# Performance work log

Measured on AMD Instinct MI355X. Metric: run time of the kernel, lower is better.

Reference implementation:

```python
import jax, jax.numpy as jnp
import numpy as np

D_MODEL = 1024
D_K = 1024
B, T = 4, 2048


def setup_inputs() -> dict:
    key = jax.random.key(0)
    kx, kq, kk, kv = jax.random.split(key, 4)
    s = 1.0 / np.sqrt(D_MODEL)
    return {
        "x": jax.random.normal(kx, (B, T, D_MODEL), dtype=jnp.float32),
        "W_q": jax.random.normal(kq, (D_MODEL, D_K), dtype=jnp.float32) * s,
        "W_k": jax.random.normal(kk, (D_MODEL, D_K), dtype=jnp.float32) * s,
        "W_v": jax.random.normal(kv, (D_MODEL, D_K), dtype=jnp.float32) * s,
    }


def reference(x, W_q, W_k, W_v):
    # x: (B, T, C); W_*: (C, d_k). Linear(no bias) == x @ W
    q = jnp.einsum('btc,ck->btk', x, W_q)
    k = jnp.einsum('btc,ck->btk', x, W_k)
    v = jnp.einsum('btc,ck->btk', x, W_v)
    d_k = W_q.shape[1]
    scores = jnp.einsum('bqk,bsk->bqs', q, k) / jnp.sqrt(jnp.asarray(d_k, x.dtype))
    T_ = x.shape[1]
    causal = jnp.tril(jnp.ones((T_, T_), dtype=bool))
    scores = jnp.where(causal, scores, jnp.asarray(-jnp.inf, scores.dtype))
    weights = jax.nn.softmax(scores, axis=-1)
    return jnp.einsum('bqs,bsk->bqk', weights, v)
```

## Files before the change

### kernel.cpp

```cpp
#include <hip/hip_runtime.h>
#include <hip/hip_bf16.h>
#include <stdint.h>

typedef __bf16 bf16x8 __attribute__((ext_vector_type(8)));
typedef float  f32x4  __attribute__((ext_vector_type(4)));
typedef unsigned int u32x4 __attribute__((ext_vector_type(4)));

__device__ __forceinline__ unsigned short f2bf(float x) {
    union { float f; unsigned u; } v; v.f = x;
    unsigned r = v.u + 0x7fffu + ((v.u >> 16) & 1u);
    return (unsigned short)(r >> 16);
}

__device__ __forceinline__ void async16(const void* g, void* l) {
    __builtin_amdgcn_global_load_lds(
        (const __attribute__((address_space(1))) void*)g,
        (__attribute__((address_space(3))) void*)l,
        16, 0, 0);
}

template <typename OutT, bool CAUSAL_SKIP, bool KLIMIT>
__global__ __launch_bounds__(256, 3) void gemm_bt(
    const unsigned short* __restrict__ A,
    const unsigned short* __restrict__ Bt,
    OutT* __restrict__ C,
    int M, int N, int K, int lda, int ldb, int ldc,
    long long sA, long long sB, long long sC, float scale)
{
    const int bn = blockIdx.x, bm = blockIdx.y, bz = blockIdx.z;
    if (CAUSAL_SKIP && bn > bm) return;

    A  += (long long)bz * sA;
    Bt += (long long)bz * sB;
    C  += (long long)bz * sC;

    const int m0 = bm * 128, n0 = bn * 128;
    const int Keff = KLIMIT ? min(K, (bm + 1) * 128) : K;

    __shared__ __align__(16) unsigned short LDS[2 * 2 * 128 * 32];

    const int tid  = threadIdx.x;
    const int w    = tid >> 6, l = tid & 63;
    const int wr   = w >> 1,  wc = w & 1;
    const int lrow = l & 15,  quad = l >> 4;

    f32x4 acc[4][4] = {};

    const int rA0  = 32 * w + (l >> 2);
    const int cOff = (((l & 3) ^ ((l >> 3) & 3))) * 8;
    const unsigned short* aG0 = A  + (long long)(m0 + rA0)      * lda + cOff;
    const unsigned short* aG1 = A  + (long long)(m0 + rA0 + 16) * lda + cOff;
    const unsigned short* bG0 = Bt + (long long)(n0 + rA0)      * ldb + cOff;
    const unsigned short* bG1 = Bt + (long long)(n0 + rA0 + 16) * ldb + cOff;
    unsigned short* aL = &LDS[(2 * w) * 512 + l * 8];
    unsigned short* bL = aL + 4096;

    const int sl = (lrow >> 1) & 3;

    async16(aG0, aL);
    async16(aG1, aL + 512);
    async16(bG0, bL);
    async16(bG1, bL + 512);

    for (int k0 = 0; k0 < Keff; k0 += 32) {
        const int cur = ((k0 >> 5) & 1) * 8192;
        __syncthreads();

        if (k0 + 32 < Keff) {
            const int nxt = cur ^ 8192;
            async16(aG0 + k0 + 32, aL + nxt);
            async16(aG1 + k0 + 32, aL + nxt + 512);
            async16(bG0 + k0 + 32, bL + nxt);
            async16(bG1 + k0 + 32, bL + nxt + 512);
        }

        const unsigned short* As = &LDS[cur];
        const unsigned short* Bs = &LDS[cur + 4096];
        bf16x8 af[4], bfr[4];
#pragma unroll
        for (int i = 0; i < 4; i++) {
            af[i]  = *(const bf16x8*)&As[(wr * 64 + i * 16 + lrow) * 32 + (quad ^ sl) * 8];
            bfr[i] = *(const bf16x8*)&Bs[(wc * 64 + i * 16 + lrow) * 32 + (quad ^ sl) * 8];
        }
#pragma unroll
        for (int i = 0; i < 4; i++)
#pragma unroll
            for (int j = 0; j < 4; j++)
                acc[i][j] = __builtin_amdgcn_mfma_f32_16x16x32_bf16(af[i], bfr[j], acc[i][j], 0, 0, 0);
    }
    __syncthreads();

    char* eb = (char*)LDS + w * 2288;
    const int erow = l >> 2, ep = l & 3;

    if constexpr (sizeof(OutT) == 2) {
#pragma unroll
        for (int i = 0; i < 4; i++) {
#pragma unroll
            for (int j = 0; j < 4; j++)
#pragma unroll
                for (int r = 0; r < 4; r++)
                    *(unsigned short*)(eb + (quad * 4 + r) * 144 + (j * 16 + lrow) * 2) =
                        f2bf(acc[i][j][r] * scale);
            const long long gm = m0 + wr * 64 + i * 16 + erow;
#pragma unroll
            for (int c = 0; c < 2; c++) {
                u32x4 d = *(u32x4*)(eb + erow * 144 + ep * 32 + c * 16);
                *(u32x4*)((unsigned short*)C + gm * ldc + (n0 + wc * 64 + ep * 16 + c * 8)) = d;
            }
        }
    } else {
#pragma unroll
        for (int i = 0; i < 4; i++) {
            const long long gm = m0 + wr * 64 + i * 16 + erow;
#pragma unroll
            for (int jc = 0; jc < 2; jc++) {
#pragma unroll
                for (int jj = 0; jj < 2; jj++)
#pragma unroll
                    for (int r = 0; r < 4; r++)
                        *(float*)(eb + (quad * 4 + r) * 144 + (jj * 16 + lrow) * 4) =
                            acc[i][2 * jc + jj][r] * scale;
#pragma unroll
                for (int c = 0; c < 2; c++) {
                    f32x4 d = *(f32x4*)(eb + erow * 144 + ep * 32 + c * 16);
                    *(f32x4*)((float*)C + gm * ldc + (n0 + wc * 64 + jc * 32 + ep * 8 + c * 4)) = d;
                }
            }
        }
    }
}

__global__ __launch_bounds__(256) void cast_f32_bf16(
    const float4* __restrict__ in, unsigned short* __restrict__ out, int n4)
{
    int i = blockIdx.x * 256 + threadIdx.x;
    if (i >= n4) return;
    float4 v = in[i];
    union { unsigned short u[4]; uint2 p; } o;
    o.u[0] = f2bf(v.x); o.u[1] = f2bf(v.y); o.u[2] = f2bf(v.z); o.u[3] = f2bf(v.w);
    *(uint2*)(out + (long long)i * 4) = o.p;
}

__global__ __launch_bounds__(256) void transpose_cast_w3(
    const float* __restrict__ W0, const float* __restrict__ W1,
    const float* __restrict__ W2, unsigned short* __restrict__ out, int n)
{
    const float* in = (blockIdx.z == 0) ? W0 : (blockIdx.z == 1) ? W1 : W2;
    out += (long long)blockIdx.z * n * n;
    __shared__ float tile[32][33];
    const int tx = threadIdx.x, ty = threadIdx.y;
    const int c0 = blockIdx.x * 32, r0 = blockIdx.y * 32;
#pragma unroll
    for (int i = 0; i < 4; i++)
        tile[ty + i * 8][tx] = in[(long long)(r0 + ty + i * 8) * n + c0 + tx];
    __syncthreads();
#pragma unroll
    for (int i = 0; i < 4; i++)
        out[(long long)(c0 + ty + i * 8) * n + r0 + tx] = f2bf(tile[tx][ty + i * 8]);
}

__global__ __launch_bounds__(256) void transpose_bf16_k(
    const unsigned short* __restrict__ in, unsigned short* __restrict__ out,
    int ldin, int ldout, long long sin, long long sout)
{
    in  += (long long)blockIdx.z * sin;
    out += (long long)blockIdx.z * sout;
    __shared__ unsigned short tile[32][33];
    const int tx = threadIdx.x, ty = threadIdx.y;
    const int c0 = blockIdx.x * 32, r0 = blockIdx.y * 32;
#pragma unroll
    for (int i = 0; i < 4; i++)
        tile[ty + i * 8][tx] = in[(long long)(r0 + ty + i * 8) * ldin + c0 + tx];
    __syncthreads();
#pragma unroll
    for (int i = 0; i < 4; i++)
        out[(long long)(c0 + ty + i * 8) * ldout + r0 + tx] = tile[tx][ty + i * 8];
}

__global__ __launch_bounds__(256) void causal_softmax(
    const float* __restrict__ S, unsigned short* __restrict__ P, int T)
{
    const int row = blockIdx.x;
    const int t   = row & (T - 1);
    const float* s = S + (long long)row * T;
    unsigned short* p = P + (long long)row * T;
    const int L = t + 1;
    const int tid = threadIdx.x;

    float v[8];
    float mx = -3.0e38f;
#pragma unroll
    for (int k = 0; k < 8; k++) {
        const int j = tid + k * 256;
        v[k] = (j < L) ? s[j] : -3.0e38f;
        mx = fmaxf(mx, v[k]);
    }
#pragma unroll
    for (int off = 32; off; off >>= 1) mx = fmaxf(mx, __shfl_xor(mx, off));
    __shared__ float red[4], red2[4];
    const int wid = tid >> 6, lid = tid & 63;
    if (lid == 0) red[wid] = mx;
    __syncthreads();
    mx = fmaxf(fmaxf(red[0], red[1]), fmaxf(red[2], red[3]));

    float sum = 0.f;
#pragma unroll
    for (int k = 0; k < 8; k++) { v[k] = __expf(v[k] - mx); sum += v[k]; }
#pragma unroll
    for (int off = 32; off; off >>= 1) sum += __shfl_xor(sum, off);
    if (lid == 0) red2[wid] = sum;
    __syncthreads();
    sum = red2[0] + red2[1] + red2[2] + red2[3];
    const float inv = 1.0f / sum;
#pragma unroll
    for (int k = 0; k < 8; k++) {
        const int j = tid + k * 256;
        p[j] = f2bf(v[k] * inv);
    }
}

extern "C" void kernel_launch(void* const* d_in, const int* in_sizes, int n_in,
                              void* d_out, int out_size, void* d_ws, size_t ws_size,
                              hipStream_t stream)
{
    const int B = 4, T = 2048, C = 1024, D = 1024;
    const float* x  = (const float*)d_in[0];
    const float* Wq = (const float*)d_in[1];
    const float* Wk = (const float*)d_in[2];
    const float* Wv = (const float*)d_in[3];
    float* out = (float*)d_out;
    char* ws = (char*)d_ws;

    const size_t MB = 1ull << 20;
    unsigned short* Xbf   = (unsigned short*)(ws + 0);
    unsigned short* WqkvT = (unsigned short*)(ws + 16 * MB);
    unsigned short* QKV   = (unsigned short*)(ws + 22 * MB);
    unsigned short* Vt    = (unsigned short*)(ws + 70 * MB);
    float*          S     = (float*)(ws + 86 * MB);
    unsigned short* P     = (unsigned short*)(ws + 0);

    const long long sX   = (long long)T * C;
    const long long sQKV = (long long)T * 3 * D;
    const long long sVt  = (long long)D * T;
    const long long sS   = (long long)T * T;
    const long long sO   = (long long)T * D;

    {
        int n4 = B * T * C / 4;
        cast_f32_bf16<<<dim3((n4 + 255) / 256), dim3(256), 0, stream>>>(
            (const float4*)x, Xbf, n4);
    }
    {
        dim3 g(32, 32, 3), b(32, 8);
        transpose_cast_w3<<<g, b, 0, stream>>>(Wq, Wk, Wv, WqkvT, 1024);
    }
    {
        dim3 g(3072 / 128, 2048 / 128, 4), b(256);
        gemm_bt<unsigned short, false, false><<<g, b, 0, stream>>>(
            Xbf, WqkvT, QKV, 2048, 3072, 1024, 1024, 1024, 3072, sX, 0, sQKV, 1.0f);
    }
    {
        dim3 g(1024 / 32, 2048 / 32, 4), b(32, 8);
        transpose_bf16_k<<<g, b, 0, stream>>>(
            QKV + 2 * D, Vt, 3 * D, T, sQKV, sVt);
    }
    {
        dim3 g(2048 / 128, 2048 / 128, 4), b(256);
        gemm_bt<float, true, false><<<g, b, 0, stream>>>(
            QKV, QKV + D, S, 2048, 2048, 1024, 3 * D, 3 * D, 2048, sQKV, sQKV, sS, 0.03125f);
    }
    {
        causal_softmax<<<dim3(B * T), dim3(256), 0, stream>>>(S, P, T);
    }
    {
        dim3 g(1024 / 128, 2048 / 128, 4), b(256);
        gemm_bt<float, false, true><<<g, b, 0, stream>>>(
            P, Vt, out, 2048, 1024, 2048, 2048, 2048, 1024, sS, sVt, sO, 1.0f);
    }
    (void)in_sizes; (void)n_in; (void)out_size; (void)ws_size;
}
```

Measured before the change: 263.2 us.

## Fold V transpose into QKV GEMM, store scores in bf16, vectorize softmax

The QKV projection GEMM now writes the V block directly in transposed layout from its accumulators, which removes the separate transpose kernel and the round trip of V through memory. Attention scores are stored as bf16 instead of fp32, halving score write and read traffic, and the softmax reads and writes 8 contiguous elements per thread as 16-byte vectors. The PV GEMM also reverses its row-block order so the heaviest causal blocks launch first. Rounding scores to bf16 before softmax loses precision, and the transposed V stores are 8-byte scattered writes.

```diff
diff --git a/kernel.cpp b/kernel.cpp
--- a/kernel.cpp
+++ b/kernel.cpp
@@ -10,6 +10,10 @@
     union { float f; unsigned u; } v; v.f = x;
     unsigned r = v.u + 0x7fffu + ((v.u >> 16) & 1u);
     return (unsigned short)(r >> 16);
+}
+
+__device__ __forceinline__ float bf2f(unsigned short b) {
+    union { unsigned u; float f; } v; v.u = ((unsigned)b) << 16; return v.f;
 }
 
 __device__ __forceinline__ void async16(const void* g, void* l) {
@@ -19,15 +23,18 @@
         16, 0, 0);
 }
 
-template <typename OutT, bool CAUSAL_SKIP, bool KLIMIT>
+template <typename OutT, bool CAUSAL_SKIP, bool KLIMIT, bool VFOLD>
 __global__ __launch_bounds__(256, 3) void gemm_bt(
     const unsigned short* __restrict__ A,
     const unsigned short* __restrict__ Bt,
     OutT* __restrict__ C,
+    unsigned short* __restrict__ VtOut,
     int M, int N, int K, int lda, int ldb, int ldc,
-    long long sA, long long sB, long long sC, float scale)
-{
-    const int bn = blockIdx.x, bm = blockIdx.y, bz = blockIdx.z;
+    int ldvt, int nsplit,
+    long long sA, long long sB, long long sC, long long sVt, float scale)
+{
+    const int bn = blockIdx.x, bz = blockIdx.z;
+    const int bm = KLIMIT ? (gridDim.y - 1 - blockIdx.y) : blockIdx.y;
     if (CAUSAL_SKIP && bn > bm) return;
 
     A  += (long long)bz * sA;
@@ -88,6 +95,26 @@
             for (int j = 0; j < 4; j++)
                 acc[i][j] = __builtin_amdgcn_mfma_f32_16x16x32_bf16(af[i], bfr[j], acc[i][j], 0, 0, 0);
     }
+
+    if constexpr (VFOLD) {
+        if (n0 >= nsplit) {
+            unsigned short* Vp = VtOut + (long long)bz * sVt;
+#pragma unroll
+            for (int i = 0; i < 4; i++) {
+                const int t = m0 + wr * 64 + i * 16 + quad * 4;
+#pragma unroll
+                for (int j = 0; j < 4; j++) {
+                    const int d = (n0 - nsplit) + wc * 64 + j * 16 + lrow;
+                    union { unsigned short u[4]; uint2 p; } o;
+#pragma unroll
+                    for (int r = 0; r < 4; r++) o.u[r] = f2bf(acc[i][j][r] * scale);
+                    *(uint2*)(Vp + (long long)d * ldvt + t) = o.p;
+                }
+            }
+            return;
+        }
+    }
+
     __syncthreads();
 
     char* eb = (char*)LDS + w * 2288;
@@ -160,40 +187,31 @@
         out[(long long)(c0 + ty + i * 8) * n + r0 + tx] = f2bf(tile[tx][ty + i * 8]);
 }
 
-__global__ __launch_bounds__(256) void transpose_bf16_k(
-    const unsigned short* __restrict__ in, unsigned short* __restrict__ out,
-    int ldin, int ldout, long long sin, long long sout)
-{
-    in  += (long long)blockIdx.z * sin;
-    out += (long long)blockIdx.z * sout;
-    __shared__ unsigned short tile[32][33];
-    const int tx = threadIdx.x, ty = threadIdx.y;
-    const int c0 = blockIdx.x * 32, r0 = blockIdx.y * 32;
-#pragma unroll
-    for (int i = 0; i < 4; i++)
-        tile[ty + i * 8][tx] = in[(long long)(r0 + ty + i * 8) * ldin + c0 + tx];
-    __syncthreads();
-#pragma unroll
-    for (int i = 0; i < 4; i++)
-        out[(long long)(c0 + ty + i * 8) * ldout + r0 + tx] = tile[tx][ty + i * 8];
-}
-
-__global__ __launch_bounds__(256) void causal_softmax(
-    const float* __restrict__ S, unsigned short* __restrict__ P, int T)
+__global__ __launch_bounds__(256) void causal_softmax_bf16(
+    const unsigned short* __restrict__ S, unsigned short* __restrict__ P, int T)
 {
     const int row = blockIdx.x;
     const int t   = row & (T - 1);
-    const float* s = S + (long long)row * T;
+    const int L   = t + 1;
+    const unsigned short* s = S + (long long)row * T;
     unsigned short* p = P + (long long)row * T;
-    const int L = t + 1;
-    const int tid = threadIdx.x;
-
+    const int tid  = threadIdx.x;
+    const int base = tid * 8;
+
+    uint4 raw = *(const uint4*)(s + base);
+    unsigned rr[4] = {raw.x, raw.y, raw.z, raw.w};
     float v[8];
+#pragma unroll
+    for (int k = 0; k < 4; k++) {
+        union { unsigned u; float f; } a, b;
+        a.u = (rr[k] & 0xFFFFu) << 16;
+        b.u = rr[k] & 0xFFFF0000u;
+        v[2 * k] = a.f; v[2 * k + 1] = b.f;
+    }
     float mx = -3.0e38f;
 #pragma unroll
     for (int k = 0; k < 8; k++) {
-        const int j = tid + k * 256;
-        v[k] = (j < L) ? s[j] : -3.0e38f;
+        if (base + k >= L) v[k] = -3.0e38f;
         mx = fmaxf(mx, v[k]);
     }
 #pragma unroll
@@ -213,11 +231,11 @@
     __syncthreads();
     sum = red2[0] + red2[1] + red2[2] + red2[3];
     const float inv = 1.0f / sum;
-#pragma unroll
-    for (int k = 0; k < 8; k++) {
-        const int j = tid + k * 256;
-        p[j] = f2bf(v[k] * inv);
-    }
+
+    union { unsigned short u[8]; uint4 q; } o;
+#pragma unroll
+    for (int k = 0; k < 8; k++) o.u[k] = f2bf(v[k] * inv);
+    *(uint4*)(p + base) = o.q;
 }
 
 extern "C" void kernel_launch(void* const* d_in, const int* in_sizes, int n_in,
@@ -235,16 +253,16 @@
     const size_t MB = 1ull << 20;
     unsigned short* Xbf   = (unsigned short*)(ws + 0);
     unsigned short* WqkvT = (unsigned short*)(ws + 16 * MB);
-    unsigned short* QKV   = (unsigned short*)(ws + 22 * MB);
-    unsigned short* Vt    = (unsigned short*)(ws + 70 * MB);
-    float*          S     = (float*)(ws + 86 * MB);
+    unsigned short* QK    = (unsigned short*)(ws + 22 * MB);
+    unsigned short* Vt    = (unsigned short*)(ws + 54 * MB);
+    unsigned short* Sbf   = (unsigned short*)(ws + 70 * MB);
     unsigned short* P     = (unsigned short*)(ws + 0);
 
-    const long long sX   = (long long)T * C;
-    const long long sQKV = (long long)T * 3 * D;
-    const long long sVt  = (long long)D * T;
-    const long long sS   = (long long)T * T;
-    const long long sO   = (long long)T * D;
+    const long long sX  = (long long)T * C;
+    const long long sQK = (long long)T * 2 * D;
+    const long long sVt = (long long)D * T;
+    const long long sS  = (long long)T * T;
+    const long long sO  = (long long)T * D;
 
     {
         int n4 = B * T * C / 4;
@@ -257,26 +275,24 @@
     }
     {
         dim3 g(3072 / 128, 2048 / 128, 4), b(256);
-        gemm_bt<unsigned short, false, false><<<g, b, 0, stream>>>(
-            Xbf, WqkvT, QKV, 2048, 3072, 1024, 1024, 1024, 3072, sX, 0, sQKV, 1.0f);
-    }
-    {
-        dim3 g(1024 / 32, 2048 / 32, 4), b(32, 8);
-        transpose_bf16_k<<<g, b, 0, stream>>>(
-            QKV + 2 * D, Vt, 3 * D, T, sQKV, sVt);
+        gemm_bt<unsigned short, false, false, true><<<g, b, 0, stream>>>(
+            Xbf, WqkvT, QK, Vt, 2048, 3072, 1024, 1024, 1024, 2048,
+             T,  2048, sX, 0, sQK, sVt, 1.0f);
     }
     {
         dim3 g(2048 / 128, 2048 / 128, 4), b(256);
-        gemm_bt<float, true, false><<<g, b, 0, stream>>>(
-            QKV, QKV + D, S, 2048, 2048, 1024, 3 * D, 3 * D, 2048, sQKV, sQKV, sS, 0.03125f);
-    }
-    {
-        causal_softmax<<<dim3(B * T), dim3(256), 0, stream>>>(S, P, T);
+        gemm_bt<unsigned short, true, false, false><<<g, b, 0, stream>>>(
+            QK, QK + D, Sbf, nullptr, 2048, 2048, 1024, 2 * D, 2 * D, 2048,
+            0, 0, sQK, sQK, sS, 0, 0.03125f);
+    }
+    {
+        causal_softmax_bf16<<<dim3(B * T), dim3(256), 0, stream>>>(Sbf, P, T);
     }
     {
         dim3 g(1024 / 128, 2048 / 128, 4), b(256);
-        gemm_bt<float, false, true><<<g, b, 0, stream>>>(
-            P, Vt, out, 2048, 1024, 2048, 2048, 2048, 1024, sS, sVt, sO, 1.0f);
+        gemm_bt<float, false, true, false><<<g, b, 0, stream>>>(
+            P, Vt, out, nullptr, 2048, 1024, 2048, 2048, 2048, 1024,
+            0, 0, sS, sVt, sO, 0, 1.0f);
     }
     (void)in_sizes; (void)n_in; (void)out_size; (void)ws_size;
 }
```

After: 251.7 us. 4.4% less time.
